# Kernel tuning notes

Measured on AMD Instinct MI355X. Metric: run time of the kernel, lower is better.

## Reference

```python
import jax, jax.numpy as jnp
import numpy as np

B, CIN, COUT, KH, KW, H, W = 32, 64, 64, 3, 3, 128, 128
STRIDE = (1, 1)
PADDING = [(1, 1), (1, 1)]


def setup_inputs() -> dict:
    key = jax.random.key(0)
    k1, k2, k3, k4 = jax.random.split(key, 4)
    x = jax.random.normal(k1, (B, CIN, H, W), dtype=jnp.float32)
    cov = jax.random.uniform(k2, (B,), dtype=jnp.float32)
    # kaiming-normal fan_out init: std = sqrt(2 / (cout*kh*kw))
    std = np.sqrt(2.0 / (COUT * KH * KW)).astype(np.float32)
    W_0 = jax.random.normal(k3, (COUT, CIN, KH, KW), dtype=jnp.float32) * std
    W_1 = jax.random.normal(k4, (COUT, CIN, KH, KW), dtype=jnp.float32) * std
    return {"x": x, "cov": cov, "W_0": W_0, "W_1": W_1}


def reference(x, cov, W_0, W_1):
    # per-sample kernel: W_0 + cov[i] * W_1  -> [B, COUT, CIN, KH, KW]
    kernels = W_0[None] + cov[:, None, None, None, None] * W_1[None]

    def conv_one(xi, k):
        # xi: [CIN, H, W], k: [COUT, CIN, KH, KW]
        out = jax.lax.conv_general_dilated(
            xi[None], k, window_strides=STRIDE, padding=PADDING,
            dimension_numbers=("NCHW", "OIHW", "NCHW"))
        return out[0]

    return jax.vmap(conv_one)(x, kernels)  # [B, COUT, H, W]
```

## Files before the change

### kernel.cpp

```cpp
#include <hip/hip_runtime.h>
#include <stdint.h>

#define B_   32
#define CIN  64
#define COUT 64
#define H_   128
#define W_   128
#define WP   130

typedef __bf16 bf16x8 __attribute__((ext_vector_type(8)));
typedef float  f32x4  __attribute__((ext_vector_type(4)));

__device__ inline unsigned int f2bf(float f) {
  union { float f; unsigned u; } uf; uf.f = f;
  unsigned u = uf.u;
  unsigned r = 0x7FFFu + ((u >> 16) & 1u);
  return (u + r) >> 16;
}

__global__ __launch_bounds__(256) void prep_w(const float* __restrict__ W0,
                                              const float* __restrict__ W1,
                                              const float* __restrict__ cov,
                                              unsigned short* __restrict__ Wb) {
  int g  = blockIdx.x * 256 + threadIdx.x;
  int ci = g & 63;
  int co = (g >> 6) & 63;
  int v  = g >> 12;
  int b  = v / 9;
  int p  = v - b * 9;
  int widx = (co * CIN + ci) * 9 + p;
  float val = W0[widx] + cov[b] * W1[widx];
  Wb[g] = (unsigned short)f2bf(val);
}

__global__ __launch_bounds__(256, 2) void conv_fused(
    const float* __restrict__ X,
    const unsigned short* __restrict__ Wb,
    float* __restrict__ out) {
  __shared__ __align__(16) unsigned short Xs[4 * WP * 64];

  int tile = blockIdx.x;
  int b  = tile >> 6;
  int h0 = (tile & 63) * 2;
  int t  = threadIdx.x;
  int wv = t >> 6;
  int l  = t & 63;

  unsigned short* dst_row = Xs + wv * WP * 64;

  {
    unsigned int* d32 = (unsigned int*)dst_row;
    if (l < 32) d32[l] = 0u;
    else        d32[129 * 32 + (l - 32)] = 0u;
  }

  int ih = h0 - 1 + wv;
  if (ih < 0 || ih > 127) {
    int4 z = {0, 0, 0, 0};
    int4* d = (int4*)(dst_row + 64);
    #pragma unroll
    for (int k = 0; k < 16; k++) d[k * 64 + l] = z;
  } else {
    const float* src = X + (((size_t)b * CIN) * H_ + ih) * W_;
    int w1 = l + 1, w2 = l + 65;
    unsigned short* p1 = dst_row + w1 * 64;
    unsigned short* p2 = dst_row + w2 * 64;
    #pragma unroll 4
    for (int ci = 0; ci < 64; ci += 2) {
      const float* s0 = src + (size_t)ci * (H_ * W_);
      float a0 = s0[l];
      float a1 = s0[H_ * W_ + l];
      float b0 = s0[64 + l];
      float b1 = s0[H_ * W_ + 64 + l];
      unsigned int lo = f2bf(a0) | (f2bf(a1) << 16);
      unsigned int hi = f2bf(b0) | (f2bf(b1) << 16);
      int blk1 = (ci >> 3) ^ (w1 & 7);
      int blk2 = (ci >> 3) ^ (w2 & 7);
      *(unsigned int*)(p1 + blk1 * 8 + (ci & 7)) = lo;
      *(unsigned int*)(p2 + blk2 * 8 + (ci & 7)) = hi;
    }
  }
  __syncthreads();

  int lh = l & 15;
  int q  = l >> 4;

  f32x4 acc[4][4];
  #pragma unroll
  for (int i = 0; i < 4; i++)
    #pragma unroll
    for (int j = 0; j < 4; j++) acc[i][j] = (f32x4){0.f, 0.f, 0.f, 0.f};

  int rbase[4], cbase[4];
  #pragma unroll
  for (int nt = 0; nt < 4; nt++) {
    int p = wv * 64 + nt * 16 + lh;
    rbase[nt] = p >> 7;
    cbase[nt] = p & 127;
  }

  const unsigned short* wbase = Wb + (size_t)b * 9 * 64 * 64;

  for (int kh = 0; kh < 3; kh++) {
    for (int kw = 0; kw < 3; kw++) {
      const unsigned short* wk = wbase + (kh * 3 + kw) * 64 * 64;
      bf16x8 af[2][4], bfr[2][4];
      #pragma unroll
      for (int ck = 0; ck < 2; ck++)
        #pragma unroll
        for (int mt = 0; mt < 4; mt++)
          af[ck][mt] = *(const bf16x8*)(wk + (mt * 16 + lh) * 64 + ck * 32 + q * 8);
      #pragma unroll
      for (int ck = 0; ck < 2; ck++)
        #pragma unroll
        for (int nt = 0; nt < 4; nt++) {
          int r = rbase[nt] + kh;
          int c = cbase[nt] + kw;
          int blk = (ck * 4 + q) ^ (c & 7);
          bfr[ck][nt] = *(const bf16x8*)(Xs + (r * WP + c) * 64 + blk * 8);
        }
      #pragma unroll
      for (int ck = 0; ck < 2; ck++)
        #pragma unroll
        for (int mt = 0; mt < 4; mt++)
          #pragma unroll
          for (int nt = 0; nt < 4; nt++)
            acc[mt][nt] = __builtin_amdgcn_mfma_f32_16x16x32_bf16(
                af[ck][mt], bfr[ck][nt], acc[mt][nt], 0, 0, 0);
    }
  }

  #pragma unroll
  for (int mt = 0; mt < 4; mt++) {
    int coutb = mt * 16 + q * 4;
    #pragma unroll
    for (int nt = 0; nt < 4; nt++) {
      int oh = h0 + rbase[nt];
      int ow = cbase[nt];
      #pragma unroll
      for (int r = 0; r < 4; r++) {
        int cout = coutb + r;
        out[(((size_t)b * COUT + cout) * H_ + oh) * W_ + ow] = acc[mt][nt][r];
      }
    }
  }
}

extern "C" void kernel_launch(void* const* d_in, const int* in_sizes, int n_in,
                              void* d_out, int out_size, void* d_ws, size_t ws_size,
                              hipStream_t stream) {
  const float* x   = (const float*)d_in[0];
  const float* cov = (const float*)d_in[1];
  const float* W0  = (const float*)d_in[2];
  const float* W1  = (const float*)d_in[3];
  float* out = (float*)d_out;

  unsigned short* Wb = (unsigned short*)d_ws;

  prep_w   <<<dim3(4608), dim3(256), 0, stream>>>(W0, W1, cov, Wb);
  conv_fused<<<dim3(2048), dim3(256), 0, stream>>>(x, Wb, out);
}
```

Before: 301.1 us.

## Split input-channel staging into two LDS phases to raise occupancy

The kernel now stages the input tile in two halves of 32 channels instead of all 64 at once. This halves the LDS footprint and allows launch bounds of 4 blocks per CU instead of 2. Staging uses float2 loads with four-channel packing and a new XOR swizzle, conversion goes through the hardware bf16 cast, and MFMA sections are wrapped in s_setprio. The cost is an extra pair of barriers and a second staging pass whose global loads are not overlapped with compute. The tighter register budget may also cause spills.

After: 308.6 us. 2.5% more time.

```diff
diff --git a/kernel.cpp b/kernel.cpp
--- a/kernel.cpp
+++ b/kernel.cpp
@@ -7,6 +7,7 @@
 #define H_   128
 #define W_   128
 #define WP   130
+#define CIH  32
 
 typedef __bf16 bf16x8 __attribute__((ext_vector_type(8)));
 typedef float  f32x4  __attribute__((ext_vector_type(4)));
@@ -16,6 +17,12 @@
   unsigned u = uf.u;
   unsigned r = 0x7FFFu + ((u >> 16) & 1u);
   return (u + r) >> 16;
+}
+
+__device__ inline unsigned int pk2(float a, float b) {
+  unsigned short x = __builtin_bit_cast(unsigned short, (__bf16)a);
+  unsigned short y = __builtin_bit_cast(unsigned short, (__bf16)b);
+  return (unsigned int)x | ((unsigned int)y << 16);
 }
 
 __global__ __launch_bounds__(256) void prep_w(const float* __restrict__ W0,
@@ -33,11 +40,51 @@
   Wb[g] = (unsigned short)f2bf(val);
 }
 
-__global__ __launch_bounds__(256, 2) void conv_fused(
+__device__ inline void stage_phase(const float* __restrict__ X,
+                                   unsigned short* dst_row,
+                                   int b, int ih, int ci0, int l, int w0,
+                                   bool first) {
+  if (first) {
+    unsigned int* d32 = (unsigned int*)dst_row;
+    if (l < 16) d32[l] = 0u;
+    else if (l < 32) d32[129 * 16 + (l - 16)] = 0u;
+  }
+  if (ih < 0 || ih > 127) {
+    if (first) {
+      int4 z = {0, 0, 0, 0};
+      int4* d = (int4*)(dst_row + CIH);
+      #pragma unroll
+      for (int k = 0; k < 8; k++) d[k * 64 + l] = z;
+    }
+    return;
+  }
+  const float* src = X + (((size_t)b * CIN + ci0) * H_ + ih) * W_ + w0;
+  const int hw = H_ * W_;
+  int wp0 = w0 + 1, wp1 = w0 + 2;
+  int sw0 = (wp0 >> 1) & 3, sw1 = (wp1 >> 1) & 3;
+  unsigned short* base0 = dst_row + wp0 * CIH;
+  unsigned short* base1 = dst_row + wp1 * CIH;
+  #pragma unroll 2
+  for (int g = 0; g < CIH; g += 4) {
+    const float* s = src + (size_t)g * hw;
+    float2 a0 = *(const float2*)(s);
+    float2 a1 = *(const float2*)(s + hw);
+    float2 a2 = *(const float2*)(s + 2 * hw);
+    float2 a3 = *(const float2*)(s + 3 * hw);
+    uint2 v0, v1;
+    v0.x = pk2(a0.x, a1.x); v0.y = pk2(a2.x, a3.x);
+    v1.x = pk2(a0.y, a1.y); v1.y = pk2(a2.y, a3.y);
+    int o = g >> 3, pos = g & 7;
+    *(uint2*)(base0 + ((o ^ sw0) << 3) + pos) = v0;
+    *(uint2*)(base1 + ((o ^ sw1) << 3) + pos) = v1;
+  }
+}
+
+__global__ __launch_bounds__(256, 4) void conv_fused(
     const float* __restrict__ X,
     const unsigned short* __restrict__ Wb,
     float* __restrict__ out) {
-  __shared__ __align__(16) unsigned short Xs[4 * WP * 64];
+  __shared__ __align__(16) unsigned short Xs[4 * WP * CIH];
 
   int tile = blockIdx.x;
   int b  = tile >> 6;
@@ -46,51 +93,12 @@
   int wv = t >> 6;
   int l  = t & 63;
 
-  unsigned short* dst_row = Xs + wv * WP * 64;
-
-  {
-    unsigned int* d32 = (unsigned int*)dst_row;
-    if (l < 32) d32[l] = 0u;
-    else        d32[129 * 32 + (l - 32)] = 0u;
-  }
-
+  unsigned short* dst_row = Xs + wv * (WP * CIH);
   int ih = h0 - 1 + wv;
-  if (ih < 0 || ih > 127) {
-    int4 z = {0, 0, 0, 0};
-    int4* d = (int4*)(dst_row + 64);
-    #pragma unroll
-    for (int k = 0; k < 16; k++) d[k * 64 + l] = z;
-  } else {
-    const float* src = X + (((size_t)b * CIN) * H_ + ih) * W_;
-    int w1 = l + 1, w2 = l + 65;
-    unsigned short* p1 = dst_row + w1 * 64;
-    unsigned short* p2 = dst_row + w2 * 64;
-    #pragma unroll 4
-    for (int ci = 0; ci < 64; ci += 2) {
-      const float* s0 = src + (size_t)ci * (H_ * W_);
-      float a0 = s0[l];
-      float a1 = s0[H_ * W_ + l];
-      float b0 = s0[64 + l];
-      float b1 = s0[H_ * W_ + 64 + l];
-      unsigned int lo = f2bf(a0) | (f2bf(a1) << 16);
-      unsigned int hi = f2bf(b0) | (f2bf(b1) << 16);
-      int blk1 = (ci >> 3) ^ (w1 & 7);
-      int blk2 = (ci >> 3) ^ (w2 & 7);
-      *(unsigned int*)(p1 + blk1 * 8 + (ci & 7)) = lo;
-      *(unsigned int*)(p2 + blk2 * 8 + (ci & 7)) = hi;
-    }
-  }
-  __syncthreads();
+  int w0 = l << 1;
 
   int lh = l & 15;
   int q  = l >> 4;
-
-  f32x4 acc[4][4];
-  #pragma unroll
-  for (int i = 0; i < 4; i++)
-    #pragma unroll
-    for (int j = 0; j < 4; j++) acc[i][j] = (f32x4){0.f, 0.f, 0.f, 0.f};
-
   int rbase[4], cbase[4];
   #pragma unroll
   for (int nt = 0; nt < 4; nt++) {
@@ -101,32 +109,47 @@
 
   const unsigned short* wbase = Wb + (size_t)b * 9 * 64 * 64;
 
-  for (int kh = 0; kh < 3; kh++) {
-    for (int kw = 0; kw < 3; kw++) {
-      const unsigned short* wk = wbase + (kh * 3 + kw) * 64 * 64;
-      bf16x8 af[2][4], bfr[2][4];
+  f32x4 acc[4][4];
+
+  stage_phase(X, dst_row, b, ih, 0, l, w0, true);
+  __syncthreads();
+
+  #pragma unroll
+  for (int i = 0; i < 4; i++)
+    #pragma unroll
+    for (int j = 0; j < 4; j++) acc[i][j] = (f32x4){0.f, 0.f, 0.f, 0.f};
+
+  #pragma unroll 1
+  for (int ph = 0; ph < 2; ph++) {
+    for (int kh = 0; kh < 3; kh++) {
       #pragma unroll
-      for (int ck = 0; ck < 2; ck++)
+      for (int kw = 0; kw < 3; kw++) {
+        const unsigned short* wk = wbase + (kh * 3 + kw) * 4096 + ph * 32;
+        bf16x8 af[4], bfr[4];
         #pragma unroll
         for (int mt = 0; mt < 4; mt++)
-          af[ck][mt] = *(const bf16x8*)(wk + (mt * 16 + lh) * 64 + ck * 32 + q * 8);
-      #pragma unroll
-      for (int ck = 0; ck < 2; ck++)
+          af[mt] = *(const bf16x8*)(wk + (mt * 16 + lh) * 64 + q * 8);
         #pragma unroll
         for (int nt = 0; nt < 4; nt++) {
           int r = rbase[nt] + kh;
           int c = cbase[nt] + kw;
-          int blk = (ck * 4 + q) ^ (c & 7);
-          bfr[ck][nt] = *(const bf16x8*)(Xs + (r * WP + c) * 64 + blk * 8);
+          int slot = q ^ ((c >> 1) & 3);
+          bfr[nt] = *(const bf16x8*)(Xs + (r * WP + c) * CIH + slot * 8);
         }
-      #pragma unroll
-      for (int ck = 0; ck < 2; ck++)
+        __builtin_amdgcn_s_setprio(1);
         #pragma unroll
         for (int mt = 0; mt < 4; mt++)
           #pragma unroll
           for (int nt = 0; nt < 4; nt++)
             acc[mt][nt] = __builtin_amdgcn_mfma_f32_16x16x32_bf16(
-                af[ck][mt], bfr[ck][nt], acc[mt][nt], 0, 0, 0);
+                af[mt], bfr[nt], acc[mt][nt], 0, 0, 0);
+        __builtin_amdgcn_s_setprio(0);
+      }
+    }
+    if (ph == 0) {
+      __syncthreads();
+      stage_phase(X, dst_row, b, ih, 32, l, w0, false);
+      __syncthreads();
     }
   }
 
```
